# Kernel tuning notes

Hardware: AMD Instinct MI355X
Metric: run time of the kernel (lower is better)

## Reference

```python
import jax, jax.numpy as jnp
import numpy as np

B, N, FIN, FOUT = 32, 1024, 128, 128
NEG_SLOPE = 0.01  # torch nn.LeakyReLU default


def setup_inputs() -> dict:
    key = jax.random.key(0)
    k1, k2, k3, k4 = jax.random.split(key, 4)
    node_mat = jax.random.normal(k1, (B, N, FIN), dtype=jnp.float32)
    adj_mat = jax.random.uniform(k2, (B, N, N), dtype=jnp.float32)
    # nn.Linear(FIN, FOUT): weight [FOUT, FIN], bias [FOUT]
    bound = 1.0 / np.sqrt(FIN)
    W = jax.random.uniform(k3, (FOUT, FIN), minval=-bound, maxval=bound, dtype=jnp.float32)
    b = jax.random.uniform(k4, (FOUT,), minval=-bound, maxval=bound, dtype=jnp.float32)
    return {"node_mat": node_mat, "adj_mat": adj_mat, "W": W, "b": b}


def reference(node_mat, adj_mat, W, b):
    # degree per node: row-sum of adjacency [B, N, 1]
    n_neighbors = adj_mat.sum(axis=-1, keepdims=True)
    # D^-1 A : the original builds eye*(1/deg) then bmm; algebraically a row scaling
    norm_adj = adj_mat / n_neighbors                      # [B, N, N]
    agg = jnp.einsum('bnm,bmf->bnf', norm_adj, node_mat)  # [B, N, FIN]
    out = jnp.einsum('bnf,of->bno', agg, W) + b           # [B, N, FOUT]
    return jnp.where(out >= 0, out, NEG_SLOPE * out)      # LeakyReLU
```

## Files before the change

### kernel.cpp

```cpp
#include <hip/hip_runtime.h>
#include <cstdint>
#include <cstddef>

#define BB   32
#define NN   1024
#define FIN  128
#define FOUT 128

typedef __attribute__((ext_vector_type(8))) short bf16x8;
typedef __attribute__((ext_vector_type(4))) float f32x4;

__device__ __forceinline__ unsigned int f2bf(float f) {
    union { float f; unsigned int u; } v; v.f = f;
    unsigned int u = v.u;
    return (u + 0x7FFFu + ((u >> 16) & 1u)) >> 16;
}
__device__ __forceinline__ unsigned int pack2(float a, float b) {
    return f2bf(a) | (f2bf(b) << 16);
}

__global__ __launch_bounds__(256) void y_kernel(const float* __restrict__ node,
                                                const float* __restrict__ W,
                                                unsigned short* __restrict__ Yt) {
    __shared__ unsigned short Wlds[128 * 136];
    __shared__ unsigned short Nlds[64 * 136];

    const int tid = threadIdx.x;
    const int bid = blockIdx.x;
    const int b   = bid >> 4;
    const int m0  = (bid & 15) * 64;

    #pragma unroll
    for (int i = 0; i < 16; ++i) {
        const int idx = i * 256 + tid;
        const int row = idx >> 5;
        const int c   = (idx & 31) * 4;
        float4 v = ((const float4*)W)[idx];
        uint2 p; p.x = pack2(v.x, v.y); p.y = pack2(v.z, v.w);
        *(uint2*)&Wlds[row * 136 + c] = p;
    }
    {
        const float* base = node + ((size_t)b * NN + m0) * FIN;
        #pragma unroll
        for (int i = 0; i < 8; ++i) {
            const int idx = i * 256 + tid;
            const int row = idx >> 5;
            const int c   = (idx & 31) * 4;
            float4 v = *(const float4*)(base + row * FIN + c);
            uint2 p; p.x = pack2(v.x, v.y); p.y = pack2(v.z, v.w);
            *(uint2*)&Nlds[row * 136 + c] = p;
        }
    }
    __syncthreads();

    const int w = tid >> 6, lane = tid & 63;
    const int wo = w * 32;
    const int lcol = lane & 15, lk = (lane >> 4) * 8;

    f32x4 acc[2][4] = {};
    #pragma unroll
    for (int kc = 0; kc < 4; ++kc) {
        const int kof = kc * 32 + lk;
        bf16x8 a[2], bb[4];
        #pragma unroll
        for (int mi = 0; mi < 2; ++mi)
            a[mi] = *(const bf16x8*)&Wlds[(wo + mi*16 + lcol) * 136 + kof];
        #pragma unroll
        for (int ni = 0; ni < 4; ++ni)
            bb[ni] = *(const bf16x8*)&Nlds[(ni*16 + lcol) * 136 + kof];
        #pragma unroll
        for (int mi = 0; mi < 2; ++mi)
            #pragma unroll
            for (int ni = 0; ni < 4; ++ni)
                acc[mi][ni] = __builtin_amdgcn_mfma_f32_16x16x32_bf16(
                    a[mi], bb[ni], acc[mi][ni], 0, 0, 0);
    }
    __syncthreads();

    unsigned short* Ylds = Wlds;
    const int rq = (lane >> 4) * 4;
    #pragma unroll
    for (int mi = 0; mi < 2; ++mi)
        #pragma unroll
        for (int ni = 0; ni < 4; ++ni)
            #pragma unroll
            for (int r = 0; r < 4; ++r) {
                const int o = wo + mi * 16 + rq + r;
                const int m = ni * 16 + lcol;
                Ylds[o * 72 + m] = (unsigned short)f2bf(acc[mi][ni][r]);
            }
    __syncthreads();

    {
        const int oq = tid >> 3, c = (tid & 7) * 8;
        #pragma unroll
        for (int j = 0; j < 4; ++j) {
            const int o = oq + 32 * j;
            uint4 v = *(const uint4*)&Ylds[o * 72 + c];
            *(uint4*)(Yt + ((size_t)b * FOUT + o) * NN + m0 + c) = v;
        }
    }
}

__global__ __launch_bounds__(256, 4) void gcn_kernel(const float* __restrict__ adj,
                                                     const unsigned short* __restrict__ Yt,
                                                     const float* __restrict__ bias,
                                                     float* __restrict__ out) {
    const int tid  = threadIdx.x;
    const int lane = tid & 63;
    const int w    = tid >> 6;
    const int bid  = blockIdx.x;
    const int b    = bid >> 5;
    const int n0   = (bid & 31) * 32;

    const int lcol = lane & 15;
    const int q    = lane >> 4;
    const int wm   = (w & 1) * 16;
    const int wn   = (w >> 1) * 64;

    const float* aRow = adj + ((size_t)(b * NN + n0 + wm + lcol)) * NN + q * 8;
    const unsigned short* bRow[4];
    #pragma unroll
    for (int ni = 0; ni < 4; ++ni)
        bRow[ni] = Yt + ((size_t)(b * FOUT + wn + ni * 16 + lcol)) * NN + q * 8;

    float bcol[4];
    #pragma unroll
    for (int ni = 0; ni < 4; ++ni) bcol[ni] = bias[wn + ni * 16 + lcol];

    f32x4 acc[4] = {};
    float rsum = 0.f;

    #pragma unroll 4
    for (int s = 0; s < 16; ++s) {
        const int k0 = s * 64;
        float4 a00 = *(const float4*)(aRow + k0);
        float4 a01 = *(const float4*)(aRow + k0 + 4);
        float4 a10 = *(const float4*)(aRow + k0 + 32);
        float4 a11 = *(const float4*)(aRow + k0 + 36);
        uint4 b0[4], b1[4];
        #pragma unroll
        for (int ni = 0; ni < 4; ++ni) {
            b0[ni] = *(const uint4*)(bRow[ni] + k0);
            b1[ni] = *(const uint4*)(bRow[ni] + k0 + 32);
        }

        rsum += ((a00.x + a00.y) + (a00.z + a00.w)) + ((a01.x + a01.y) + (a01.z + a01.w));
        rsum += ((a10.x + a10.y) + (a10.z + a10.w)) + ((a11.x + a11.y) + (a11.z + a11.w));

        uint4 pk0, pk1;
        pk0.x = pack2(a00.x, a00.y); pk0.y = pack2(a00.z, a00.w);
        pk0.z = pack2(a01.x, a01.y); pk0.w = pack2(a01.z, a01.w);
        pk1.x = pack2(a10.x, a10.y); pk1.y = pack2(a10.z, a10.w);
        pk1.z = pack2(a11.x, a11.y); pk1.w = pack2(a11.z, a11.w);
        const bf16x8 af0 = *(const bf16x8*)&pk0;
        const bf16x8 af1 = *(const bf16x8*)&pk1;

        #pragma unroll
        for (int ni = 0; ni < 4; ++ni)
            acc[ni] = __builtin_amdgcn_mfma_f32_16x16x32_bf16(
                af0, *(const bf16x8*)&b0[ni], acc[ni], 0, 0, 0);
        #pragma unroll
        for (int ni = 0; ni < 4; ++ni)
            acc[ni] = __builtin_amdgcn_mfma_f32_16x16x32_bf16(
                af1, *(const bf16x8*)&b1[ni], acc[ni], 0, 0, 0);
    }

    rsum += __shfl_xor(rsum, 16);
    rsum += __shfl_xor(rsum, 32);

    float sc[4];
    #pragma unroll
    for (int r = 0; r < 4; ++r) sc[r] = 1.0f / __shfl(rsum, q * 4 + r);

    float* outB = out + ((size_t)(b * NN + n0 + wm)) * FOUT + wn;
    #pragma unroll
    for (int ni = 0; ni < 4; ++ni) {
        #pragma unroll
        for (int r = 0; r < 4; ++r) {
            float v = acc[ni][r] * sc[r] + bcol[ni];
            v = (v >= 0.f) ? v : 0.01f * v;
            outB[(size_t)(q * 4 + r) * FOUT + ni * 16 + lcol] = v;
        }
    }
}

extern "C" void kernel_launch(void* const* d_in, const int* in_sizes, int n_in,
                              void* d_out, int out_size, void* d_ws, size_t ws_size,
                              hipStream_t stream) {
    const float* node = (const float*)d_in[0];
    const float* adj  = (const float*)d_in[1];
    const float* W    = (const float*)d_in[2];
    const float* bias = (const float*)d_in[3];
    float* out = (float*)d_out;
    unsigned short* Yt = (unsigned short*)d_ws;

    hipLaunchKernelGGL(y_kernel,   dim3(512),  dim3(256), 0, stream, node, W, Yt);
    hipLaunchKernelGGL(gcn_kernel, dim3(1024), dim3(256), 0, stream, adj, Yt, bias, out);
}
```

Measured before the change: 271.3 us.

## Stage adjacency and Yt tiles through LDS with direct global-to-LDS loads

```diff
diff --git a/kernel.cpp b/kernel.cpp
--- a/kernel.cpp
+++ b/kernel.cpp
@@ -17,6 +17,12 @@
 }
 __device__ __forceinline__ unsigned int pack2(float a, float b) {
     return f2bf(a) | (f2bf(b) << 16);
+}
+
+__device__ __forceinline__ void load_lds16(const void* g, void* l) {
+    __builtin_amdgcn_global_load_lds(
+        (const __attribute__((address_space(1))) unsigned int*)g,
+        (__attribute__((address_space(3))) unsigned int*)l, 16, 0, 0);
 }
 
 __global__ __launch_bounds__(256) void y_kernel(const float* __restrict__ node,
@@ -102,68 +108,66 @@
     }
 }
 
-__global__ __launch_bounds__(256, 4) void gcn_kernel(const float* __restrict__ adj,
-                                                     const unsigned short* __restrict__ Yt,
-                                                     const float* __restrict__ bias,
-                                                     float* __restrict__ out) {
+__global__ __launch_bounds__(256) void gcn_kernel(const float* __restrict__ adj,
+                                                  const unsigned short* __restrict__ Yt,
+                                                  const float* __restrict__ bias,
+                                                  float* __restrict__ out) {
+    __shared__ char smem[10240];
+
     const int tid  = threadIdx.x;
     const int lane = tid & 63;
     const int w    = tid >> 6;
     const int bid  = blockIdx.x;
-    const int b    = bid >> 5;
-    const int n0   = (bid & 31) * 32;
+    const int b    = bid >> 6;
+    const int n0   = (bid & 63) * 16;
 
     const int lcol = lane & 15;
     const int q    = lane >> 4;
-    const int wm   = (w & 1) * 16;
-    const int wn   = (w >> 1) * 64;
-
-    const float* aRow = adj + ((size_t)(b * NN + n0 + wm + lcol)) * NN + q * 8;
-    const unsigned short* bRow[4];
-    #pragma unroll
-    for (int ni = 0; ni < 4; ++ni)
-        bRow[ni] = Yt + ((size_t)(b * FOUT + wn + ni * 16 + lcol)) * NN + q * 8;
-
-    float bcol[4];
-    #pragma unroll
-    for (int ni = 0; ni < 4; ++ni) bcol[ni] = bias[wn + ni * 16 + lcol];
-
-    f32x4 acc[4] = {};
+    const int wn   = w * 32;
+
+    const float* aSrc = adj
+        + ((size_t)(b * NN + n0 + (lane & 15))) * NN
+        + ((w & 1) * 4 + (lane >> 4)) * 4;
+    char* aDst = smem + (w & 1) * 1024;
+
+    const unsigned short* bSrc = Yt
+        + ((size_t)(b * FOUT + (w & 1) * 64 + lane)) * NN
+        + (w >> 1) * 8;
+    char* bDst1 = smem + 2048 + w * 1024;
+    char* bDst2 = smem + 2048 + (w + 4) * 1024;
+
+    const float bcol0 = bias[wn + lcol];
+    const float bcol1 = bias[wn + 16 + lcol];
+
+    f32x4 acc0 = {}, acc1 = {};
     float rsum = 0.f;
 
-    #pragma unroll 4
-    for (int s = 0; s < 16; ++s) {
-        const int k0 = s * 64;
-        float4 a00 = *(const float4*)(aRow + k0);
-        float4 a01 = *(const float4*)(aRow + k0 + 4);
-        float4 a10 = *(const float4*)(aRow + k0 + 32);
-        float4 a11 = *(const float4*)(aRow + k0 + 36);
-        uint4 b0[4], b1[4];
-        #pragma unroll
-        for (int ni = 0; ni < 4; ++ni) {
-            b0[ni] = *(const uint4*)(bRow[ni] + k0);
-            b1[ni] = *(const uint4*)(bRow[ni] + k0 + 32);
-        }
-
-        rsum += ((a00.x + a00.y) + (a00.z + a00.w)) + ((a01.x + a01.y) + (a01.z + a01.w));
-        rsum += ((a10.x + a10.y) + (a10.z + a10.w)) + ((a11.x + a11.y) + (a11.z + a11.w));
-
-        uint4 pk0, pk1;
-        pk0.x = pack2(a00.x, a00.y); pk0.y = pack2(a00.z, a00.w);
-        pk0.z = pack2(a01.x, a01.y); pk0.w = pack2(a01.z, a01.w);
-        pk1.x = pack2(a10.x, a10.y); pk1.y = pack2(a10.z, a10.w);
-        pk1.z = pack2(a11.x, a11.y); pk1.w = pack2(a11.z, a11.w);
-        const bf16x8 af0 = *(const bf16x8*)&pk0;
-        const bf16x8 af1 = *(const bf16x8*)&pk1;
-
-        #pragma unroll
-        for (int ni = 0; ni < 4; ++ni)
-            acc[ni] = __builtin_amdgcn_mfma_f32_16x16x32_bf16(
-                af0, *(const bf16x8*)&b0[ni], acc[ni], 0, 0, 0);
-        #pragma unroll
-        for (int ni = 0; ni < 4; ++ni)
-            acc[ni] = __builtin_amdgcn_mfma_f32_16x16x32_bf16(
-                af1, *(const bf16x8*)&b1[ni], acc[ni], 0, 0, 0);
+    const char* aF0 = smem + q * 512 + lcol * 16;
+    const char* aF1 = aF0 + 256;
+    const char* bF0 = smem + 2048 + q * 2048 + (wn + lcol) * 16;
+    const char* bF1 = bF0 + 256;
+
+    for (int s = 0; s < 32; ++s) {
+        if (w < 2) load_lds16(aSrc, aDst);
+        load_lds16(bSrc,      bDst1);
+        load_lds16(bSrc + 16, bDst2);
+        __syncthreads();
+
+        const float4 fa0 = *(const float4*)aF0;
+        const float4 fa1 = *(const float4*)aF1;
+        rsum += ((fa0.x + fa0.y) + (fa0.z + fa0.w))
+              + ((fa1.x + fa1.y) + (fa1.z + fa1.w));
+        uint4 pk;
+        pk.x = pack2(fa0.x, fa0.y); pk.y = pack2(fa0.z, fa0.w);
+        pk.z = pack2(fa1.x, fa1.y); pk.w = pack2(fa1.z, fa1.w);
+        const bf16x8 af  = *(const bf16x8*)&pk;
+        const bf16x8 bf0 = *(const bf16x8*)bF0;
+        const bf16x8 bf1 = *(const bf16x8*)bF1;
+        acc0 = __builtin_amdgcn_mfma_f32_16x16x32_bf16(af, bf0, acc0, 0, 0, 0);
+        acc1 = __builtin_amdgcn_mfma_f32_16x16x32_bf16(af, bf1, acc1, 0, 0, 0);
+        __syncthreads();
+
+        aSrc += 32; bSrc += 32;
     }
 
     rsum += __shfl_xor(rsum, 16);
@@ -173,15 +177,16 @@
     #pragma unroll
     for (int r = 0; r < 4; ++r) sc[r] = 1.0f / __shfl(rsum, q * 4 + r);
 
-    float* outB = out + ((size_t)(b * NN + n0 + wm)) * FOUT + wn;
-    #pragma unroll
-    for (int ni = 0; ni < 4; ++ni) {
-        #pragma unroll
-        for (int r = 0; r < 4; ++r) {
-            float v = acc[ni][r] * sc[r] + bcol[ni];
-            v = (v >= 0.f) ? v : 0.01f * v;
-            outB[(size_t)(q * 4 + r) * FOUT + ni * 16 + lcol] = v;
-        }
+    float* outB = out + ((size_t)(b * NN + n0)) * FOUT;
+    #pragma unroll
+    for (int r = 0; r < 4; ++r) {
+        const int row = q * 4 + r;
+        float v0 = acc0[r] * sc[r] + bcol0;
+        float v1 = acc1[r] * sc[r] + bcol1;
+        v0 = (v0 >= 0.f) ? v0 : 0.01f * v0;
+        v1 = (v1 >= 0.f) ? v1 : 0.01f * v1;
+        outB[(size_t)row * FOUT + wn + lcol]      = v0;
+        outB[(size_t)row * FOUT + wn + 16 + lcol] = v1;
     }
 }
 
@@ -196,5 +201,5 @@
     unsigned short* Yt = (unsigned short*)d_ws;
 
     hipLaunchKernelGGL(y_kernel,   dim3(512),  dim3(256), 0, stream, node, W, Yt);
-    hipLaunchKernelGGL(gcn_kernel, dim3(1024), dim3(256), 0, stream, adj, Yt, bias, out);
-}
+    hipLaunchKernelGGL(gcn_kernel, dim3(2048), dim3(256), 0, stream, adj, Yt, bias, out);
+}
```

Result: slower. 311.4 us (+14.8%).
